# Performance work log

Measured on AMD Instinct MI355X. Metric: run time of the kernel, lower is better.

The kernel has to match this reference:

```python
import jax, jax.numpy as jnp
import numpy as np

N = 50000        # nodes
DEG = 32         # in-degree per node
E = N * DEG      # edges
T = 4            # towers
NODE = 128       # node_dim
OUT = 128        # out_dim
IN_T = NODE // T   # 32, divide_input tower slice
OUT_T = OUT // T   # 32
AVG_D_LOG = float(np.log(5.0))  # avg_d = {'log': log(4+1)}
EPS = 1e-5


def setup_inputs() -> dict:
    key = jax.random.key(0)
    ks = jax.random.split(key, 6)
    h = jax.random.normal(ks[0], (N, NODE), jnp.float32)
    src = jax.random.randint(ks[1], (E,), 0, N)
    # every node gets exactly DEG incoming edges (sorted dst)
    dst = jnp.repeat(jnp.arange(N), DEG)
    # per-tower pretrans MLP (1 layer): Linear(2*IN_T -> OUT_T)
    W_pre = jax.random.normal(ks[2], (T, 2 * IN_T, OUT_T), jnp.float32) * 0.05
    b_pre = jnp.zeros((T, OUT_T), jnp.float32)
    # per-tower posttrans MLP (1 layer): Linear(12*OUT_T + IN_T -> OUT_T)
    W_post = jax.random.normal(ks[3], (T, 12 * OUT_T + IN_T, OUT_T), jnp.float32) * 0.05
    b_post = jnp.zeros((T, OUT_T), jnp.float32)
    # mixing network: Linear(OUT -> OUT) + LeakyReLU
    W_mix = jax.random.normal(ks[4], (OUT, OUT), jnp.float32) * 0.05
    b_mix = jnp.zeros((OUT,), jnp.float32)
    return dict(h=h, src=src, dst=dst, W_pre=W_pre, b_pre=b_pre,
                W_post=W_post, b_post=b_post, W_mix=W_mix, b_mix=b_mix)


def _pna_forward(h, src, dst, W_pre, b_pre, W_post, b_post, W_mix, b_mix):
    ht = h.reshape(N, T, IN_T)                    # divide_input: tower slices
    z2 = jnp.concatenate([ht[src], ht[dst]], axis=-1)   # [E,T,2*IN_T] (src||dst)
    # pretrans: MLP(1 layer) then ReLU
    e = jax.nn.relu(jnp.einsum('etk,tko->eto', z2, W_pre) + b_pre)  # [E,T,OUT_T]

    deg = jax.ops.segment_sum(jnp.ones((E,), h.dtype), dst, num_segments=N)  # [N]
    deg_c = jnp.maximum(deg, 1.0)[:, None, None]
    seg = lambda x: jax.ops.segment_sum(x, dst, num_segments=N)
    mean = seg(e) / deg_c                          # [N,T,OUT_T]
    mean_sq = seg(e * e) / deg_c
    std = jnp.sqrt(jax.nn.relu(mean_sq - mean * mean) + EPS)
    mx = jax.ops.segment_max(e, dst, num_segments=N)
    mn = jax.ops.segment_min(e, dst, num_segments=N)
    agg = jnp.concatenate([mean, mx, mn, std], axis=-1)   # [N,T,4*OUT_T]

    # scalers: identity, amplification, attenuation (D = in-degree)
    sc = jnp.log(deg + 1.0) / AVG_D_LOG            # [N]
    amp = agg * sc[:, None, None]
    att = agg / jnp.maximum(sc, EPS)[:, None, None]
    h_agg = jnp.concatenate([agg, amp, att], axis=-1)     # [N,T,12*OUT_T]

    # posttrans: cat(h_tower, aggregated) -> MLP(1 layer) -> ReLU
    z = jnp.concatenate([ht, h_agg], axis=-1)      # [N,T,IN_T+12*OUT_T]
    hp = jax.nn.relu(jnp.einsum('ntk,tko->nto', z, W_post) + b_post)  # [N,T,OUT_T]
    h_cat = hp.reshape(N, OUT)

    h_out = jax.nn.leaky_relu(h_cat @ W_mix + b_mix, 0.01)
    return h + h_out                               # residual (node_dim == out_dim)


def reference(h, src, dst, W_pre, b_pre, W_post, b_post, W_mix, b_mix):
    return _pna_forward(h, src, dst, W_pre, b_pre, W_post, b_post, W_mix, b_mix)
```

## Files before the change

kernel.cpp:

```cpp
#include <hip/hip_runtime.h>
#include <hip/hip_bf16.h>
#include <math.h>

#define N_NODES 50000
#define DEG     32
#define NBP     40
#define NBF     16
#define EPSV    1e-5f

typedef __attribute__((ext_vector_type(8))) short short8;
typedef __attribute__((ext_vector_type(4))) float f32x4;

__global__ void k_prep(const float* __restrict__ W_post, const float* __restrict__ W_mix,
                       __hip_bfloat16* __restrict__ WeffT, __hip_bfloat16* __restrict__ WmixT,
                       float sc, float isc) {
    int i = blockIdx.x * 256 + threadIdx.x;
    if (i < 4 * 32 * 160) {
        int k = i % 160, to = i / 160, o = to & 31, t = to >> 5;
        const float* Wt = W_post + t * 416 * 32;
        float v;
        if (k < 32) v = Wt[k * 32 + o];
        else {
            int g = k - 32;
            v = Wt[(32 + g) * 32 + o] + sc * Wt[(160 + g) * 32 + o] + isc * Wt[(288 + g) * 32 + o];
        }
        WeffT[i] = __float2bfloat16(v);
    }
    int j = i - 4 * 32 * 160;
    if (j >= 0 && j < 128 * 128) {
        int k = j & 127, o = j >> 7;
        WmixT[j] = __float2bfloat16(W_mix[k * 128 + o]);
    }
}

__global__ __launch_bounds__(256) void k_proj(const float* __restrict__ h,
        const float* __restrict__ W_pre, const float* __restrict__ b_pre,
        __hip_bfloat16* __restrict__ Pd, __hip_bfloat16* __restrict__ Ps) {
    int tid = threadIdx.x;
    int c = tid & 127, half = tid >> 7;
    int t = c >> 5, o = c & 31;
    const float* Wt = W_pre + t * 64 * 32 + half * 32 * 32;
    float wr[32];
#pragma unroll
    for (int k = 0; k < 32; ++k) wr[k] = Wt[k * 32 + o];
    float bp = half ? b_pre[t * 32 + o] : 0.f;
    __shared__ float sh[8][128];
    int base = blockIdx.x * NBP;
    for (int r = 0; r < NBP / 8; ++r) {
        int n0 = base + r * 8;
        __syncthreads();
        ((float4*)sh)[tid] = ((const float4*)(h + n0 * 128))[tid];
        __syncthreads();
        float acc[8];
#pragma unroll
        for (int ni = 0; ni < 8; ++ni) {
            const float4* h4 = (const float4*)(&sh[ni][t * 32]);
            float a = 0.f;
#pragma unroll
            for (int k4 = 0; k4 < 8; ++k4) {
                float4 hv = h4[k4];
                a = fmaf(hv.x, wr[4*k4+0], a);
                a = fmaf(hv.y, wr[4*k4+1], a);
                a = fmaf(hv.z, wr[4*k4+2], a);
                a = fmaf(hv.w, wr[4*k4+3], a);
            }
            acc[ni] = a;
        }
#pragma unroll
        for (int ni = 0; ni < 8; ++ni) {
            int n = n0 + ni;
            if (half) Pd[n * 128 + c] = __float2bfloat16(acc[ni] + bp);
            else      Ps[n * 128 + c] = __float2bfloat16(acc[ni]);
        }
    }
}

__global__ __launch_bounds__(256) void k_fused(const float* __restrict__ h,
        const int* __restrict__ src, const __hip_bfloat16* __restrict__ Pd,
        const __hip_bfloat16* __restrict__ Ps, const __hip_bfloat16* __restrict__ WeffT,
        const __hip_bfloat16* __restrict__ WmixT, const float* __restrict__ b_post,
        const float* __restrict__ b_mix, float* __restrict__ out) {
    __shared__ __align__(16) __hip_bfloat16 sZ[NBF][648];
    __shared__ __align__(16) __hip_bfloat16 sHp[NBF][136];
    int tid = threadIdx.x, w = tid >> 6, lane = tid & 63;
    int nb = blockIdx.x * NBF;

    int c0 = 2 * lane;
    int tA = c0 >> 5, oA = c0 & 31;
#pragma unroll
    for (int r = 0; r < 4; ++r) {
        int row = r * 4 + w;
        int n = nb + row;
        int vsrc = src[n * DEG + (lane & 31)];
        float2 hv = *(const float2*)(h + n * 128 + c0);
        unsigned int pdu = *(const unsigned int*)(Pd + n * 128 + c0);
        float pd0 = __uint_as_float(pdu << 16);
        float pd1 = __uint_as_float(pdu & 0xffff0000u);
        float sum0 = 0.f, sum1 = 0.f, sq0 = 0.f, sq1 = 0.f;
        float mx0 = -1e30f, mx1 = -1e30f, mn0 = 1e30f, mn1 = 1e30f;
#pragma unroll
        for (int j0 = 0; j0 < DEG; j0 += 8) {
            unsigned int pv[8];
#pragma unroll
            for (int u = 0; u < 8; ++u) {
                int s = __builtin_amdgcn_readlane(vsrc, j0 + u);
                pv[u] = *(const unsigned int*)(Ps + s * 128 + c0);
            }
#pragma unroll
            for (int u = 0; u < 8; ++u) {
                float f0 = __uint_as_float(pv[u] << 16);
                float f1 = __uint_as_float(pv[u] & 0xffff0000u);
                float e0 = fmaxf(f0 + pd0, 0.f);
                float e1 = fmaxf(f1 + pd1, 0.f);
                sum0 += e0; sq0 = fmaf(e0, e0, sq0);
                mx0 = fmaxf(mx0, e0); mn0 = fminf(mn0, e0);
                sum1 += e1; sq1 = fmaf(e1, e1, sq1);
                mx1 = fmaxf(mx1, e1); mn1 = fminf(mn1, e1);
            }
        }
        float mean0 = sum0 * (1.f / DEG), mean1 = sum1 * (1.f / DEG);
        float sd0 = sqrtf(fmaxf(sq0 * (1.f / DEG) - mean0 * mean0, 0.f) + EPSV);
        float sd1 = sqrtf(fmaxf(sq1 * (1.f / DEG) - mean1 * mean1, 0.f) + EPSV);
        unsigned int* zr = (unsigned int*)(&sZ[row][tA * 160 + oA]);
        auto pack = [](float a, float b) {
            return (unsigned int)(__bfloat16_as_ushort(__float2bfloat16(a))) |
                   ((unsigned int)(__bfloat16_as_ushort(__float2bfloat16(b))) << 16);
        };
        zr[0]  = pack(hv.x, hv.y);
        zr[16] = pack(mean0, mean1);
        zr[32] = pack(mx0, mx1);
        zr[48] = pack(mn0, mn1);
        zr[64] = pack(sd0, sd1);
    }
    __syncthreads();

    int col = lane & 15, quad = lane >> 4;
#pragma unroll
    for (int i = 0; i < 2; ++i) {
        int ct = w * 2 + i, t = ct >> 1, nt = ct & 1;
        f32x4 acc = {0.f, 0.f, 0.f, 0.f};
        int oc = t * 32 + nt * 16 + col;
        const __hip_bfloat16* wrow = WeffT + oc * 160 + quad * 8;
#pragma unroll
        for (int ks = 0; ks < 5; ++ks) {
            short8 a = *(const short8*)(&sZ[col][t * 160 + ks * 32 + quad * 8]);
            short8 b = *(const short8*)(wrow + ks * 32);
            acc = __builtin_amdgcn_mfma_f32_16x16x32_bf16(a, b, acc, 0, 0, 0);
        }
        float bp = b_post[oc];
#pragma unroll
        for (int r = 0; r < 4; ++r)
            sHp[quad * 4 + r][oc] = __float2bfloat16(fmaxf(acc[r] + bp, 0.f));
    }
    __syncthreads();

#pragma unroll
    for (int i = 0; i < 2; ++i) {
        int nt = w * 2 + i;
        f32x4 acc = {0.f, 0.f, 0.f, 0.f};
        int oc = nt * 16 + col;
        const __hip_bfloat16* wrow = WmixT + oc * 128 + quad * 8;
#pragma unroll
        for (int ks = 0; ks < 4; ++ks) {
            short8 a = *(const short8*)(&sHp[col][ks * 32 + quad * 8]);
            short8 b = *(const short8*)(wrow + ks * 32);
            acc = __builtin_amdgcn_mfma_f32_16x16x32_bf16(a, b, acc, 0, 0, 0);
        }
        float bm = b_mix[oc];
#pragma unroll
        for (int r = 0; r < 4; ++r) {
            int n = nb + quad * 4 + r;
            float m = acc[r] + bm;
            m = m > 0.f ? m : 0.01f * m;
            out[n * 128 + oc] = h[n * 128 + oc] + m;
        }
    }
}

extern "C" void kernel_launch(void* const* d_in, const int* in_sizes, int n_in,
                              void* d_out, int out_size, void* d_ws, size_t ws_size,
                              hipStream_t stream) {
    const float* h      = (const float*)d_in[0];
    const int*   src    = (const int*)d_in[1];
    const float* W_pre  = (const float*)d_in[3];
    const float* b_pre  = (const float*)d_in[4];
    const float* W_post = (const float*)d_in[5];
    const float* b_post = (const float*)d_in[6];
    const float* W_mix  = (const float*)d_in[7];
    const float* b_mix  = (const float*)d_in[8];
    float* out = (float*)d_out;

    char* ws = (char*)d_ws;
    __hip_bfloat16* WeffT = (__hip_bfloat16*)ws;
    __hip_bfloat16* WmixT = (__hip_bfloat16*)(ws + 40960);
    __hip_bfloat16* Pd    = (__hip_bfloat16*)(ws + 73728);
    __hip_bfloat16* Ps    = (__hip_bfloat16*)(ws + 73728 + 12800000);

    double scd = log(33.0) / log(5.0);
    float sc = (float)scd, isc = (float)(1.0 / scd);

    hipLaunchKernelGGL(k_prep, dim3(144), dim3(256), 0, stream, W_post, W_mix, WeffT, WmixT, sc, isc);
    hipLaunchKernelGGL(k_proj, dim3(N_NODES / NBP), dim3(256), 0, stream, h, W_pre, b_pre, Pd, Ps);
    hipLaunchKernelGGL(k_fused, dim3(N_NODES / NBF), dim3(256), 0, stream,
                       h, src, Pd, Ps, WeffT, WmixT, b_post, b_mix, out);
}
```

Before: 178.6 us.

## Move pretrans projection to bf16 MFMA and vectorize gather statistics

The per-tower pretrans projection kernel is rewritten to convert h tiles to bf16 in shared memory and compute Pd/Ps with 16x16x32 bf16 MFMA, replacing the scalar fp32 FMA loop. A transposed bf16 copy of W_pre is prepared in the prep kernel. The gather loop in the fused kernel now issues 16 loads per batch instead of 8 and uses 2-wide float vectors for the statistics, aiming for packed math and more memory-level parallelism. The projection input is rounded to bf16, which reduces precision of the pre-activation messages.

```diff
diff --git a/kernel.cpp b/kernel.cpp
--- a/kernel.cpp
+++ b/kernel.cpp
@@ -4,18 +4,19 @@
 
 #define N_NODES 50000
 #define DEG     32
-#define NBP     40
 #define NBF     16
 #define EPSV    1e-5f
 
 typedef __attribute__((ext_vector_type(8))) short short8;
 typedef __attribute__((ext_vector_type(4))) float f32x4;
+typedef __attribute__((ext_vector_type(2))) float f32x2;
 
 __global__ void k_prep(const float* __restrict__ W_post, const float* __restrict__ W_mix,
+                       const float* __restrict__ W_pre,
                        __hip_bfloat16* __restrict__ WeffT, __hip_bfloat16* __restrict__ WmixT,
-                       float sc, float isc) {
+                       __hip_bfloat16* __restrict__ WpreT, float sc, float isc) {
     int i = blockIdx.x * 256 + threadIdx.x;
-    if (i < 4 * 32 * 160) {
+    if (i < 20480) {
         int k = i % 160, to = i / 160, o = to & 31, t = to >> 5;
         const float* Wt = W_post + t * 416 * 32;
         float v;
@@ -25,52 +26,66 @@
             v = Wt[(32 + g) * 32 + o] + sc * Wt[(160 + g) * 32 + o] + isc * Wt[(288 + g) * 32 + o];
         }
         WeffT[i] = __float2bfloat16(v);
-    }
-    int j = i - 4 * 32 * 160;
-    if (j >= 0 && j < 128 * 128) {
+    } else if (i < 36864) {
+        int j = i - 20480;
         int k = j & 127, o = j >> 7;
         WmixT[j] = __float2bfloat16(W_mix[k * 128 + o]);
+    } else if (i < 45056) {
+        int q = i - 36864;
+        int k = q & 31, o = (q >> 5) & 31, p = q >> 10;
+        int t = p >> 1, half = p & 1;
+        WpreT[q] = __float2bfloat16(W_pre[t * 2048 + (half * 32 + k) * 32 + o]);
     }
 }
 
 __global__ __launch_bounds__(256) void k_proj(const float* __restrict__ h,
-        const float* __restrict__ W_pre, const float* __restrict__ b_pre,
+        const __hip_bfloat16* __restrict__ WpreT, const float* __restrict__ b_pre,
         __hip_bfloat16* __restrict__ Pd, __hip_bfloat16* __restrict__ Ps) {
-    int tid = threadIdx.x;
-    int c = tid & 127, half = tid >> 7;
-    int t = c >> 5, o = c & 31;
-    const float* Wt = W_pre + t * 64 * 32 + half * 32 * 32;
-    float wr[32];
-#pragma unroll
-    for (int k = 0; k < 32; ++k) wr[k] = Wt[k * 32 + o];
-    float bp = half ? b_pre[t * 32 + o] : 0.f;
-    __shared__ float sh[8][128];
-    int base = blockIdx.x * NBP;
-    for (int r = 0; r < NBP / 8; ++r) {
-        int n0 = base + r * 8;
-        __syncthreads();
-        ((float4*)sh)[tid] = ((const float4*)(h + n0 * 128))[tid];
-        __syncthreads();
-        float acc[8];
-#pragma unroll
-        for (int ni = 0; ni < 8; ++ni) {
-            const float4* h4 = (const float4*)(&sh[ni][t * 32]);
-            float a = 0.f;
-#pragma unroll
-            for (int k4 = 0; k4 < 8; ++k4) {
-                float4 hv = h4[k4];
-                a = fmaf(hv.x, wr[4*k4+0], a);
-                a = fmaf(hv.y, wr[4*k4+1], a);
-                a = fmaf(hv.z, wr[4*k4+2], a);
-                a = fmaf(hv.w, wr[4*k4+3], a);
+    __shared__ __align__(16) __hip_bfloat16 sA[64][136];
+    int tid = threadIdx.x, w = tid >> 6, lane = tid & 63;
+    int nb = blockIdx.x * 64;
+
+    int colc = (tid & 31) * 4, rowb = tid >> 5;
+#pragma unroll
+    for (int i = 0; i < 8; ++i) {
+        int row = i * 8 + rowb;
+        int n = nb + row;
+        unsigned int lo = 0, hi = 0;
+        if (n < N_NODES) {
+            float4 f = *(const float4*)(h + n * 128 + colc);
+            lo = (unsigned int)__bfloat16_as_ushort(__float2bfloat16(f.x)) |
+                 ((unsigned int)__bfloat16_as_ushort(__float2bfloat16(f.y)) << 16);
+            hi = (unsigned int)__bfloat16_as_ushort(__float2bfloat16(f.z)) |
+                 ((unsigned int)__bfloat16_as_ushort(__float2bfloat16(f.w)) << 16);
+        }
+        *(uint2*)(&sA[row][colc]) = make_uint2(lo, hi);
+    }
+    __syncthreads();
+
+    int col = lane & 15, quad = lane >> 4;
+    int r0 = w * 16;
+    short8 a[4];
+#pragma unroll
+    for (int t = 0; t < 4; ++t)
+        a[t] = *(const short8*)(&sA[r0 + col][t * 32 + quad * 8]);
+
+#pragma unroll
+    for (int p = 0; p < 8; ++p) {
+        int t = p >> 1, isPd = p & 1;
+#pragma unroll
+        for (int ct = 0; ct < 2; ++ct) {
+            int o = ct * 16 + col;
+            short8 b = *(const short8*)(WpreT + p * 1024 + o * 32 + quad * 8);
+            f32x4 acc = {0.f, 0.f, 0.f, 0.f};
+            acc = __builtin_amdgcn_mfma_f32_16x16x32_bf16(a[t], b, acc, 0, 0, 0);
+            float bp = isPd ? b_pre[t * 32 + o] : 0.f;
+            __hip_bfloat16* dst = (isPd ? Pd : Ps);
+#pragma unroll
+            for (int r = 0; r < 4; ++r) {
+                int n = nb + r0 + quad * 4 + r;
+                if (n < N_NODES)
+                    dst[n * 128 + t * 32 + o] = __float2bfloat16(acc[r] + bp);
             }
-            acc[ni] = a;
-        }
-#pragma unroll
-        for (int ni = 0; ni < 8; ++ni) {
-            int n = n0 + ni;
-            if (half) Pd[n * 128 + c] = __float2bfloat16(acc[ni] + bp);
-            else      Ps[n * 128 + c] = __float2bfloat16(acc[ni]);
         }
     }
 }
@@ -87,6 +102,7 @@
 
     int c0 = 2 * lane;
     int tA = c0 >> 5, oA = c0 & 31;
+    const f32x2 zero2 = {0.f, 0.f};
 #pragma unroll
     for (int r = 0; r < 4; ++r) {
         int row = r * 4 + w;
@@ -94,42 +110,41 @@
         int vsrc = src[n * DEG + (lane & 31)];
         float2 hv = *(const float2*)(h + n * 128 + c0);
         unsigned int pdu = *(const unsigned int*)(Pd + n * 128 + c0);
-        float pd0 = __uint_as_float(pdu << 16);
-        float pd1 = __uint_as_float(pdu & 0xffff0000u);
-        float sum0 = 0.f, sum1 = 0.f, sq0 = 0.f, sq1 = 0.f;
-        float mx0 = -1e30f, mx1 = -1e30f, mn0 = 1e30f, mn1 = 1e30f;
-#pragma unroll
-        for (int j0 = 0; j0 < DEG; j0 += 8) {
-            unsigned int pv[8];
-#pragma unroll
-            for (int u = 0; u < 8; ++u) {
+        f32x2 pd2 = {__uint_as_float(pdu << 16), __uint_as_float(pdu & 0xffff0000u)};
+        f32x2 sum = zero2, sq = zero2;
+        f32x2 mx = {-1e30f, -1e30f}, mn = {1e30f, 1e30f};
+#pragma unroll
+        for (int j0 = 0; j0 < DEG; j0 += 16) {
+            unsigned int pv[16];
+#pragma unroll
+            for (int u = 0; u < 16; ++u) {
                 int s = __builtin_amdgcn_readlane(vsrc, j0 + u);
                 pv[u] = *(const unsigned int*)(Ps + s * 128 + c0);
             }
 #pragma unroll
-            for (int u = 0; u < 8; ++u) {
-                float f0 = __uint_as_float(pv[u] << 16);
-                float f1 = __uint_as_float(pv[u] & 0xffff0000u);
-                float e0 = fmaxf(f0 + pd0, 0.f);
-                float e1 = fmaxf(f1 + pd1, 0.f);
-                sum0 += e0; sq0 = fmaf(e0, e0, sq0);
-                mx0 = fmaxf(mx0, e0); mn0 = fminf(mn0, e0);
-                sum1 += e1; sq1 = fmaf(e1, e1, sq1);
-                mx1 = fmaxf(mx1, e1); mn1 = fminf(mn1, e1);
+            for (int u = 0; u < 16; ++u) {
+                f32x2 f = {__uint_as_float(pv[u] << 16),
+                           __uint_as_float(pv[u] & 0xffff0000u)};
+                f32x2 e = __builtin_elementwise_max(f + pd2, zero2);
+                sum += e;
+                sq = e * e + sq;
+                mx = __builtin_elementwise_max(mx, e);
+                mn = __builtin_elementwise_min(mn, e);
             }
         }
-        float mean0 = sum0 * (1.f / DEG), mean1 = sum1 * (1.f / DEG);
-        float sd0 = sqrtf(fmaxf(sq0 * (1.f / DEG) - mean0 * mean0, 0.f) + EPSV);
-        float sd1 = sqrtf(fmaxf(sq1 * (1.f / DEG) - mean1 * mean1, 0.f) + EPSV);
+        f32x2 mean = sum * (1.f / DEG);
+        f32x2 var = sq * (1.f / DEG) - mean * mean;
+        float sd0 = sqrtf(fmaxf(var.x, 0.f) + EPSV);
+        float sd1 = sqrtf(fmaxf(var.y, 0.f) + EPSV);
         unsigned int* zr = (unsigned int*)(&sZ[row][tA * 160 + oA]);
         auto pack = [](float a, float b) {
             return (unsigned int)(__bfloat16_as_ushort(__float2bfloat16(a))) |
                    ((unsigned int)(__bfloat16_as_ushort(__float2bfloat16(b))) << 16);
         };
         zr[0]  = pack(hv.x, hv.y);
-        zr[16] = pack(mean0, mean1);
-        zr[32] = pack(mx0, mx1);
-        zr[48] = pack(mn0, mn1);
+        zr[16] = pack(mean.x, mean.y);
+        zr[32] = pack(mx.x, mx.y);
+        zr[48] = pack(mn.x, mn.y);
         zr[64] = pack(sd0, sd1);
     }
     __syncthreads();
@@ -193,14 +208,17 @@
     char* ws = (char*)d_ws;
     __hip_bfloat16* WeffT = (__hip_bfloat16*)ws;
     __hip_bfloat16* WmixT = (__hip_bfloat16*)(ws + 40960);
-    __hip_bfloat16* Pd    = (__hip_bfloat16*)(ws + 73728);
-    __hip_bfloat16* Ps    = (__hip_bfloat16*)(ws + 73728 + 12800000);
+    __hip_bfloat16* WpreT = (__hip_bfloat16*)(ws + 73728);
+    __hip_bfloat16* Pd    = (__hip_bfloat16*)(ws + 90112);
+    __hip_bfloat16* Ps    = (__hip_bfloat16*)(ws + 90112 + 12800000);
 
     double scd = log(33.0) / log(5.0);
     float sc = (float)scd, isc = (float)(1.0 / scd);
 
-    hipLaunchKernelGGL(k_prep, dim3(144), dim3(256), 0, stream, W_post, W_mix, WeffT, WmixT, sc, isc);
-    hipLaunchKernelGGL(k_proj, dim3(N_NODES / NBP), dim3(256), 0, stream, h, W_pre, b_pre, Pd, Ps);
+    hipLaunchKernelGGL(k_prep, dim3(176), dim3(256), 0, stream,
+                       W_post, W_mix, W_pre, WeffT, WmixT, WpreT, sc, isc);
+    hipLaunchKernelGGL(k_proj, dim3((N_NODES + 63) / 64), dim3(256), 0, stream,
+                       h, WpreT, b_pre, Pd, Ps);
     hipLaunchKernelGGL(k_fused, dim3(N_NODES / NBF), dim3(256), 0, stream,
                        h, src, Pd, Ps, WeffT, WmixT, b_post, b_mix, out);
 }
```

New measurement: 171.6 us. 3.9% less time.
